# Performance work log

Hardware: AMD Instinct MI355X
Metric: run time of the kernel (lower is better)

Reference implementation:

```python
import jax, jax.numpy as jnp
import numpy as np

B, D_IN, D_H, W_RANK, U_RANK = 8192, 1024, 2048, 256, 256


def setup_inputs() -> dict:
    key = jax.random.key(0)
    ks = jax.random.split(key, 6)
    return {
        "input": jax.random.normal(ks[0], (B, D_IN), dtype=jnp.float32),
        "state": jax.random.normal(ks[1], (B, D_H), dtype=jnp.float32),
        "W1": 0.1 * jax.random.normal(ks[2], (W_RANK, D_IN), dtype=jnp.float32),
        "W2": 0.1 * jax.random.normal(ks[3], (D_H, W_RANK), dtype=jnp.float32),
        "U1": 0.1 * jax.random.normal(ks[4], (U_RANK, D_H), dtype=jnp.float32),
        "U2": 0.1 * jax.random.normal(ks[5], (D_H, U_RANK), dtype=jnp.float32),
        "bias_gate": jnp.ones((1, D_H), dtype=jnp.float32),
        "bias_update": jnp.ones((1, D_H), dtype=jnp.float32),
        "zeta": 1.0 * jnp.ones((1, 1), dtype=jnp.float32),
        "nu": -4.0 * jnp.ones((1, 1), dtype=jnp.float32),
    }


def reference(input, state, W1, W2, U1, U2, bias_gate, bias_update, zeta, nu):
    # Low-rank projections: Wx = x @ W1^T @ W2^T ; Uh = h @ U1^T @ U2^T
    wx = jnp.einsum("bi,ri->br", input, W1)          # [B, wRank]
    wx = jnp.einsum("br,hr->bh", wx, W2)             # [B, H]
    uh = jnp.einsum("bh,rh->br", state, U1)          # [B, uRank]
    uh = jnp.einsum("br,hr->bh", uh, U2)             # [B, H]
    pre = wx + uh                                     # shared pre-activation
    z = jax.nn.sigmoid(pre + bias_gate)               # gate (sigmoid)
    h_cand = jnp.tanh(pre + bias_update)              # update (tanh)
    # h_t = z*h_{t-1} + (sigmoid(zeta)*(1-z) + sigmoid(nu)) * h_cand
    new_h = z * state + (jax.nn.sigmoid(zeta) * (1.0 - z) + jax.nn.sigmoid(nu)) * h_cand
    return new_h
```

## Files before the change

### kernel.cpp

```cpp
#include <hip/hip_runtime.h>
#include <hip/hip_fp16.h>
#include <cstdint>
#include <cstddef>


typedef _Float16 half8 __attribute__((ext_vector_type(8)));
typedef float f32x4 __attribute__((ext_vector_type(4)));

#define DIN 1024
#define DH 2048
#define RK 256
#define RBLD 768
#define OFF_W1H 0
#define OFF_U1H 262144
#define OFF_W2H 786432
#define OFF_U2H 1310720
#define WB_HALVES 1835008

__device__ __forceinline__ half8 cvt8(const float4 a, const float4 b) {
  half8 h;
  h[0] = (_Float16)a.x; h[1] = (_Float16)a.y; h[2] = (_Float16)a.z; h[3] = (_Float16)a.w;
  h[4] = (_Float16)b.x; h[5] = (_Float16)b.y; h[6] = (_Float16)b.z; h[7] = (_Float16)b.w;
  return h;
}

__global__ __launch_bounds__(256)
void fgrnn_prep(const float* __restrict__ W1, const float* __restrict__ U1,
                const float* __restrict__ W2, const float* __restrict__ U2,
                _Float16* __restrict__ wb) {
  const int q = blockIdx.x * 256 + threadIdx.x;
  const float* src;
  int rel;
  if (q < 65536) { src = W1; rel = q; }
  else if (q < 196608) { src = U1; rel = q - 65536; }
  else if (q < 327680) { src = W2; rel = q - 196608; }
  else { src = U2; rel = q - 327680; }
  const float4 v = reinterpret_cast<const float4*>(src)[rel];
  union { _Float16 h[4]; uint2 u; } cv;
  cv.h[0] = (_Float16)v.x; cv.h[1] = (_Float16)v.y;
  cv.h[2] = (_Float16)v.z; cv.h[3] = (_Float16)v.w;
  reinterpret_cast<uint2*>(wb)[q] = cv.u;
}

template <int MI>
__device__ __forceinline__ void s1_body(
    const float* __restrict__ A, const int KA, const int kbase,
    const _Float16* __restrict__ Bw, _Float16* __restrict__ rbuf,
    const int row0, const int colbase,
    _Float16* __restrict__ AsBase, _Float16* __restrict__ BsBase) {
  constexpr int APASS = MI / 2;
  constexpr int ASTRIDE = MI * 32 * 64;
  constexpr int BSTRIDE = 256 * 64;

  const int tid = threadIdx.x;
  const int lane = tid & 63;
  const int w = tid >> 6;
  const int wr = w >> 2, wc = w & 3;
  const int sr = tid >> 3;
  const int sc = (tid & 7) * 8;

  f32x4 acc[MI][4];
#pragma unroll
  for (int i = 0; i < MI; ++i)
#pragma unroll
    for (int j = 0; j < 4; ++j) acc[i][j] = (f32x4){0.f, 0.f, 0.f, 0.f};

  float4 raE[APASS][2], raO[APASS][2];
  half8 rbE[4], rbO[4];

  auto LOADG = [&](float4 (&ra)[APASS][2], half8 (&rb)[4], int it) {
    const int k0 = kbase + it * 64;
#pragma unroll
    for (int j = 0; j < APASS; ++j) {
      const float* s = A + (size_t)(row0 + j * 64 + sr) * KA + k0 + sc;
      ra[j][0] = *reinterpret_cast<const float4*>(s);
      ra[j][1] = *reinterpret_cast<const float4*>(s + 4);
    }
#pragma unroll
    for (int j = 0; j < 4; ++j)
      rb[j] = *reinterpret_cast<const half8*>(Bw + (size_t)(j * 64 + sr) * KA + k0 + sc);
  };
  auto STORE = [&](const float4 (&ra)[APASS][2], const half8 (&rb)[4],
                   _Float16* as, _Float16* bs) {
#pragma unroll
    for (int j = 0; j < APASS; ++j) {
      const int r = j * 64 + sr;
      *reinterpret_cast<half8*>(&as[r * 64 + (sc ^ ((r & 7) << 3))]) =
          cvt8(ra[j][0], ra[j][1]);
    }
#pragma unroll
    for (int j = 0; j < 4; ++j) {
      const int r = j * 64 + sr;
      *reinterpret_cast<half8*>(&bs[r * 64 + (sc ^ ((r & 7) << 3))]) = rb[j];
    }
  };
  auto COMPUTE = [&](const _Float16* as, const _Float16* bs) {
#pragma unroll
    for (int kk = 0; kk < 64; kk += 32) {
      half8 af[MI], bf[4];
#pragma unroll
      for (int mi = 0; mi < MI; ++mi) {
        const int r = wr * (MI * 16) + mi * 16 + (lane & 15);
        af[mi] = *reinterpret_cast<const half8*>(
            &as[r * 64 + ((kk + 8 * (lane >> 4)) ^ ((r & 7) << 3))]);
      }
#pragma unroll
      for (int ni = 0; ni < 4; ++ni) {
        const int r = wc * 64 + ni * 16 + (lane & 15);
        bf[ni] = *reinterpret_cast<const half8*>(
            &bs[r * 64 + ((kk + 8 * (lane >> 4)) ^ ((r & 7) << 3))]);
      }
#pragma unroll
      for (int mi = 0; mi < MI; ++mi)
#pragma unroll
        for (int ni = 0; ni < 4; ++ni)
          acc[mi][ni] =
              __builtin_amdgcn_mfma_f32_16x16x32_f16(af[mi], bf[ni], acc[mi][ni], 0, 0, 0);
    }
  };
  auto BAR = [&]() {
    asm volatile("s_waitcnt lgkmcnt(0)" ::: "memory");
    __builtin_amdgcn_s_barrier();
    asm volatile("" ::: "memory");
  };

  _Float16* as0 = AsBase;
  _Float16* as1 = AsBase + ASTRIDE;
  _Float16* bs0 = BsBase;
  _Float16* bs1 = BsBase + BSTRIDE;

  LOADG(raE, rbE, 0);
  LOADG(raO, rbO, 1);
  STORE(raE, rbE, as0, bs0);
  BAR();

#pragma unroll 1
  for (int it2 = 0; it2 < 16; it2 += 2) {
    if (it2 + 2 < 16) LOADG(raE, rbE, it2 + 2);
    COMPUTE(as0, bs0);
    STORE(raO, rbO, as1, bs1);
    BAR();
    if (it2 + 3 < 16) LOADG(raO, rbO, it2 + 3);
    COMPUTE(as1, bs1);
    if (it2 + 2 < 16) STORE(raE, rbE, as0, bs0);
    BAR();
  }

#pragma unroll
  for (int mi = 0; mi < MI; ++mi)
#pragma unroll
    for (int ni = 0; ni < 4; ++ni)
#pragma unroll
      for (int e = 0; e < 4; ++e) {
        const int row = row0 + wr * (MI * 16) + mi * 16 + 4 * (lane >> 4) + e;
        const int col = colbase + wc * 64 + ni * 16 + (lane & 15);
        rbuf[(size_t)row * RBLD + col] = (_Float16)acc[mi][ni][e];
      }
}

__global__ __launch_bounds__(512)
void fgrnn_stage1(const float* __restrict__ x, const float* __restrict__ h,
                  const _Float16* __restrict__ wb, _Float16* __restrict__ rbuf) {
  __shared__ _Float16 As[2 * 128 * 64];
  __shared__ _Float16 Bs[2 * 256 * 64];
  const int bid = blockIdx.x;
  if (bid < 128) {
    s1_body<2>(x, DIN, 0, wb + OFF_W1H, rbuf, bid * 64, 0, As, Bs);
  } else if (bid < 192) {
    s1_body<4>(h, DH, 0, wb + OFF_U1H, rbuf, (bid - 128) * 128, 256, As, Bs);
  } else {
    s1_body<4>(h, DH, 1024, wb + OFF_U1H, rbuf, (bid - 192) * 128, 512, As, Bs);
  }
}

__global__ __launch_bounds__(256)
void fgrnn_stage2(const _Float16* __restrict__ rbuf, const _Float16* __restrict__ wb,
                  const float* __restrict__ state,
                  const float* __restrict__ bg, const float* __restrict__ bu,
                  const float* __restrict__ zeta, const float* __restrict__ nu,
                  float* __restrict__ out) {
  const int bid = blockIdx.x;
  const int L = (bid & 7) * 256 + (bid >> 3);
  const int mtile = L >> 4;
  const int ntile = L & 15;
  const int row0 = mtile * 64;
  const int col0 = ntile * 128;
  const _Float16* W2h = wb + OFF_W2H;
  const _Float16* U2h = wb + OFF_U2H;

  __shared__ _Float16 As[64 * 64];
  __shared__ _Float16 Bs[128 * 64];

  const int tid = threadIdx.x;
  const int lane = tid & 63;
  const int w = tid >> 6;
  const int wr = w >> 1, wc = w & 1;

  f32x4 acc[2][4];
#pragma unroll
  for (int i = 0; i < 2; ++i)
#pragma unroll
    for (int j = 0; j < 4; ++j) acc[i][j] = (f32x4){0.f, 0.f, 0.f, 0.f};

  const int sr = tid >> 3;
  const int sc = (tid & 7) * 8;

  half8 pa[2], pa2[2], pb[4];

  auto LOADG = [&](int it) {
    const int k0 = it * 64;
    const bool iswx = (k0 < 256);
#pragma unroll
    for (int j = 0; j < 2; ++j) {
      const _Float16* p = rbuf + (size_t)(row0 + j * 32 + sr) * RBLD + k0 + sc;
      pa[j] = *reinterpret_cast<const half8*>(p);
      if (!iswx) pa2[j] = *reinterpret_cast<const half8*>(p + 256);
    }
    const _Float16* Bh = iswx ? W2h : U2h;
    const int kb = k0 & 255;
#pragma unroll
    for (int j = 0; j < 4; ++j)
      pb[j] = *reinterpret_cast<const half8*>(Bh + (size_t)(col0 + j * 32 + sr) * RK + kb + sc);
  };
  auto STORE = [&](int it) {
    const int k0 = it * 64;
#pragma unroll
    for (int j = 0; j < 2; ++j) {
      half8 v = pa[j];
      if (k0 >= 256) v = v + pa2[j];
      const int r = j * 32 + sr;
      *reinterpret_cast<half8*>(&As[r * 64 + (sc ^ ((r & 7) << 3))]) = v;
    }
#pragma unroll
    for (int j = 0; j < 4; ++j) {
      const int r = j * 32 + sr;
      *reinterpret_cast<half8*>(&Bs[r * 64 + (sc ^ ((r & 7) << 3))]) = pb[j];
    }
  };

  LOADG(0);
  STORE(0);
  __syncthreads();

  for (int it = 0; it < 8; ++it) {
    const bool more = (it + 1 < 8);
    if (more) LOADG(it + 1);
#pragma unroll
    for (int kk = 0; kk < 64; kk += 32) {
      half8 af[2], bf[4];
#pragma unroll
      for (int mi = 0; mi < 2; ++mi) {
        const int r = wr * 32 + mi * 16 + (lane & 15);
        af[mi] = *reinterpret_cast<const half8*>(
            &As[r * 64 + ((kk + 8 * (lane >> 4)) ^ ((r & 7) << 3))]);
      }
#pragma unroll
      for (int ni = 0; ni < 4; ++ni) {
        const int r = wc * 64 + ni * 16 + (lane & 15);
        bf[ni] = *reinterpret_cast<const half8*>(
            &Bs[r * 64 + ((kk + 8 * (lane >> 4)) ^ ((r & 7) << 3))]);
      }
#pragma unroll
      for (int mi = 0; mi < 2; ++mi)
#pragma unroll
        for (int ni = 0; ni < 4; ++ni)
          acc[mi][ni] =
              __builtin_amdgcn_mfma_f32_16x16x32_f16(af[mi], bf[ni], acc[mi][ni], 0, 0, 0);
    }
    if (more) {
      __syncthreads();
      STORE(it + 1);
    }
    __syncthreads();
  }

  const float LOG2E = 1.44269504f;
  const float sz = __builtin_amdgcn_rcpf(1.f + __builtin_amdgcn_exp2f(-zeta[0] * LOG2E));
  const float sn = __builtin_amdgcn_rcpf(1.f + __builtin_amdgcn_exp2f(-nu[0] * LOG2E));
#pragma unroll
  for (int mi = 0; mi < 2; ++mi)
#pragma unroll
    for (int ni = 0; ni < 4; ++ni) {
      const int col = col0 + wc * 64 + ni * 16 + (lane & 15);
      const float bgc = bg[col];
      const float buc = bu[col];
#pragma unroll
      for (int e = 0; e < 4; ++e) {
        const int row = row0 + wr * 32 + mi * 16 + 4 * (lane >> 4) + e;
        const float pre = acc[mi][ni][e];
        const float zg =
            __builtin_amdgcn_rcpf(1.f + __builtin_amdgcn_exp2f(-(pre + bgc) * LOG2E));
        const float hc =
            1.f - 2.f * __builtin_amdgcn_rcpf(
                            1.f + __builtin_amdgcn_exp2f((pre + buc) * (2.f * LOG2E)));
        const float sv = state[(size_t)row * DH + col];
        out[(size_t)row * DH + col] = zg * sv + (sz * (1.f - zg) + sn) * hc;
      }
    }
}

extern "C" void kernel_launch(void* const* d_in, const int* in_sizes, int n_in,
                              void* d_out, int out_size, void* d_ws, size_t ws_size,
                              hipStream_t stream) {
  const float* input = (const float*)d_in[0];
  const float* state = (const float*)d_in[1];
  const float* W1 = (const float*)d_in[2];
  const float* W2 = (const float*)d_in[3];
  const float* U1 = (const float*)d_in[4];
  const float* U2 = (const float*)d_in[5];
  const float* bg = (const float*)d_in[6];
  const float* bu = (const float*)d_in[7];
  const float* zeta = (const float*)d_in[8];
  const float* nu = (const float*)d_in[9];
  float* out = (float*)d_out;

  _Float16* rbuf = (_Float16*)d_ws;
  _Float16* wb = rbuf + (size_t)8192 * RBLD;

  fgrnn_prep<<<1792, 256, 0, stream>>>(W1, U1, W2, U2, wb);
  fgrnn_stage1<<<256, 512, 0, stream>>>(input, state, wb, rbuf);
  fgrnn_stage2<<<2048, 256, 0, stream>>>(rbuf, wb, state, bg, bu, zeta, nu, out);
}
```

Before: 69.03 us.

## Retile stage-1 GEMM into uniform 64x128 tiles with more, smaller blocks

Stage 1 previously ran 256 blocks of 512 threads, and their tiles were unequal in size (64-row blocks for x, 128-row blocks for h). It now launches 768 uniform 256-thread blocks, each computing a 64x128 output tile. A swizzled block index groups blocks across XCDs. The aim is to fill all CUs evenly and allow several blocks per CU, at the cost of re-reading the A rows once per 128-column half.

```diff
diff --git a/kernel.cpp b/kernel.cpp
--- a/kernel.cpp
+++ b/kernel.cpp
@@ -15,7 +15,6 @@
 #define OFF_U1H 262144
 #define OFF_W2H 786432
 #define OFF_U2H 1310720
-#define WB_HALVES 1835008
 
 __device__ __forceinline__ half8 cvt8(const float4 a, const float4 b) {
   half8 h;
@@ -42,65 +41,75 @@
   reinterpret_cast<uint2*>(wb)[q] = cv.u;
 }
 
-template <int MI>
-__device__ __forceinline__ void s1_body(
-    const float* __restrict__ A, const int KA, const int kbase,
-    const _Float16* __restrict__ Bw, _Float16* __restrict__ rbuf,
-    const int row0, const int colbase,
-    _Float16* __restrict__ AsBase, _Float16* __restrict__ BsBase) {
-  constexpr int APASS = MI / 2;
-  constexpr int ASTRIDE = MI * 32 * 64;
-  constexpr int BSTRIDE = 256 * 64;
+__global__ __launch_bounds__(256, 3)
+void fgrnn_stage1(const float* __restrict__ x, const float* __restrict__ h,
+                  const _Float16* __restrict__ wb, _Float16* __restrict__ rbuf) {
+  __shared__ _Float16 As[2 * 64 * 64];
+  __shared__ _Float16 Bs[2 * 128 * 64];
+
+  const int bid = blockIdx.x;
+  const int L = (bid & 7) * 96 + (bid >> 3);
+  const int g = L >> 8;
+  const int rem = L & 255;
+  const int ncol = rem >> 7;
+  const int mtile = rem & 127;
+  const bool isx = (g == 0);
+  const float* A = isx ? x : h;
+  const int KA = isx ? DIN : DH;
+  const int kbase = (g == 2) ? 1024 : 0;
+  const _Float16* Bw = wb + (isx ? OFF_W1H : OFF_U1H) + (size_t)(ncol * 128) * KA;
+  const int row0 = mtile * 64;
+  const int colbase = g * 256 + ncol * 128;
 
   const int tid = threadIdx.x;
   const int lane = tid & 63;
   const int w = tid >> 6;
-  const int wr = w >> 2, wc = w & 3;
+  const int wr = w >> 1, wc = w & 1;
   const int sr = tid >> 3;
   const int sc = (tid & 7) * 8;
 
-  f32x4 acc[MI][4];
-#pragma unroll
-  for (int i = 0; i < MI; ++i)
+  f32x4 acc[2][4];
+#pragma unroll
+  for (int i = 0; i < 2; ++i)
 #pragma unroll
     for (int j = 0; j < 4; ++j) acc[i][j] = (f32x4){0.f, 0.f, 0.f, 0.f};
 
-  float4 raE[APASS][2], raO[APASS][2];
+  float4 raE[2][2], raO[2][2];
   half8 rbE[4], rbO[4];
 
-  auto LOADG = [&](float4 (&ra)[APASS][2], half8 (&rb)[4], int it) {
+  auto LOADG = [&](float4 (&ra)[2][2], half8 (&rb)[4], int it) {
     const int k0 = kbase + it * 64;
 #pragma unroll
-    for (int j = 0; j < APASS; ++j) {
-      const float* s = A + (size_t)(row0 + j * 64 + sr) * KA + k0 + sc;
+    for (int j = 0; j < 2; ++j) {
+      const float* s = A + (size_t)(row0 + j * 32 + sr) * KA + k0 + sc;
       ra[j][0] = *reinterpret_cast<const float4*>(s);
       ra[j][1] = *reinterpret_cast<const float4*>(s + 4);
     }
 #pragma unroll
     for (int j = 0; j < 4; ++j)
-      rb[j] = *reinterpret_cast<const half8*>(Bw + (size_t)(j * 64 + sr) * KA + k0 + sc);
-  };
-  auto STORE = [&](const float4 (&ra)[APASS][2], const half8 (&rb)[4],
+      rb[j] = *reinterpret_cast<const half8*>(Bw + (size_t)(j * 32 + sr) * KA + k0 + sc);
+  };
+  auto STORE = [&](const float4 (&ra)[2][2], const half8 (&rb)[4],
                    _Float16* as, _Float16* bs) {
 #pragma unroll
-    for (int j = 0; j < APASS; ++j) {
-      const int r = j * 64 + sr;
+    for (int j = 0; j < 2; ++j) {
+      const int r = j * 32 + sr;
       *reinterpret_cast<half8*>(&as[r * 64 + (sc ^ ((r & 7) << 3))]) =
           cvt8(ra[j][0], ra[j][1]);
     }
 #pragma unroll
     for (int j = 0; j < 4; ++j) {
-      const int r = j * 64 + sr;
+      const int r = j * 32 + sr;
       *reinterpret_cast<half8*>(&bs[r * 64 + (sc ^ ((r & 7) << 3))]) = rb[j];
     }
   };
   auto COMPUTE = [&](const _Float16* as, const _Float16* bs) {
 #pragma unroll
     for (int kk = 0; kk < 64; kk += 32) {
-      half8 af[MI], bf[4];
-#pragma unroll
-      for (int mi = 0; mi < MI; ++mi) {
-        const int r = wr * (MI * 16) + mi * 16 + (lane & 15);
+      half8 af[2], bf[4];
+#pragma unroll
+      for (int mi = 0; mi < 2; ++mi) {
+        const int r = wr * 32 + mi * 16 + (lane & 15);
         af[mi] = *reinterpret_cast<const half8*>(
             &as[r * 64 + ((kk + 8 * (lane >> 4)) ^ ((r & 7) << 3))]);
       }
@@ -111,7 +120,7 @@
             &bs[r * 64 + ((kk + 8 * (lane >> 4)) ^ ((r & 7) << 3))]);
       }
 #pragma unroll
-      for (int mi = 0; mi < MI; ++mi)
+      for (int mi = 0; mi < 2; ++mi)
 #pragma unroll
         for (int ni = 0; ni < 4; ++ni)
           acc[mi][ni] =
@@ -124,10 +133,10 @@
     asm volatile("" ::: "memory");
   };
 
-  _Float16* as0 = AsBase;
-  _Float16* as1 = AsBase + ASTRIDE;
-  _Float16* bs0 = BsBase;
-  _Float16* bs1 = BsBase + BSTRIDE;
+  _Float16* as0 = As;
+  _Float16* as1 = As + 64 * 64;
+  _Float16* bs0 = Bs;
+  _Float16* bs1 = Bs + 128 * 64;
 
   LOADG(raE, rbE, 0);
   LOADG(raO, rbO, 1);
@@ -147,30 +156,15 @@
   }
 
 #pragma unroll
-  for (int mi = 0; mi < MI; ++mi)
+  for (int mi = 0; mi < 2; ++mi)
 #pragma unroll
     for (int ni = 0; ni < 4; ++ni)
 #pragma unroll
       for (int e = 0; e < 4; ++e) {
-        const int row = row0 + wr * (MI * 16) + mi * 16 + 4 * (lane >> 4) + e;
+        const int row = row0 + wr * 32 + mi * 16 + 4 * (lane >> 4) + e;
         const int col = colbase + wc * 64 + ni * 16 + (lane & 15);
         rbuf[(size_t)row * RBLD + col] = (_Float16)acc[mi][ni][e];
       }
-}
-
-__global__ __launch_bounds__(512)
-void fgrnn_stage1(const float* __restrict__ x, const float* __restrict__ h,
-                  const _Float16* __restrict__ wb, _Float16* __restrict__ rbuf) {
-  __shared__ _Float16 As[2 * 128 * 64];
-  __shared__ _Float16 Bs[2 * 256 * 64];
-  const int bid = blockIdx.x;
-  if (bid < 128) {
-    s1_body<2>(x, DIN, 0, wb + OFF_W1H, rbuf, bid * 64, 0, As, Bs);
-  } else if (bid < 192) {
-    s1_body<4>(h, DH, 0, wb + OFF_U1H, rbuf, (bid - 128) * 128, 256, As, Bs);
-  } else {
-    s1_body<4>(h, DH, 1024, wb + OFF_U1H, rbuf, (bid - 192) * 128, 512, As, Bs);
-  }
 }
 
 __global__ __launch_bounds__(256)
@@ -318,6 +312,6 @@
   _Float16* wb = rbuf + (size_t)8192 * RBLD;
 
   fgrnn_prep<<<1792, 256, 0, stream>>>(W1, U1, W2, U2, wb);
-  fgrnn_stage1<<<256, 512, 0, stream>>>(input, state, wb, rbuf);
+  fgrnn_stage1<<<768, 256, 0, stream>>>(input, state, wb, rbuf);
   fgrnn_stage2<<<2048, 256, 0, stream>>>(rbuf, wb, state, bg, bu, zeta, nu, out);
 }
```

Measured after the change: 78.64 us. 1.14x slower.

## Use direct global-to-LDS loads for weights and double-buffer both GEMM stages

Applied to the files above, without the earlier changes.

Weight tiles in both stages now go straight from global memory into LDS through global_load_lds, so they no longer pass through registers. Stage 2 gains double-buffered LDS with one barrier per iteration in place of two syncthreads. Stage 1 is retiled so each block covers 128 output columns over more rows (8 waves laid out 4x2), and the register pipeline is simplified to a single buffer. Wave priority is raised around the MFMA compute. The aim is less register pressure and fewer stalls on loads and barriers, but each iteration now waits on vmcnt(0), which may expose global load latency.

```diff
diff --git a/kernel.cpp b/kernel.cpp
--- a/kernel.cpp
+++ b/kernel.cpp
@@ -15,13 +15,18 @@
 #define OFF_U1H 262144
 #define OFF_W2H 786432
 #define OFF_U2H 1310720
-#define WB_HALVES 1835008
 
 __device__ __forceinline__ half8 cvt8(const float4 a, const float4 b) {
   half8 h;
   h[0] = (_Float16)a.x; h[1] = (_Float16)a.y; h[2] = (_Float16)a.z; h[3] = (_Float16)a.w;
   h[4] = (_Float16)b.x; h[5] = (_Float16)b.y; h[6] = (_Float16)b.z; h[7] = (_Float16)b.w;
   return h;
+}
+
+__device__ __forceinline__ void gload16(const _Float16* g, _Float16* lds) {
+  __builtin_amdgcn_global_load_lds(
+      (const __attribute__((address_space(1))) unsigned*)g,
+      (__attribute__((address_space(3))) unsigned*)lds, 16, 0, 0);
 }
 
 __global__ __launch_bounds__(256)
@@ -47,15 +52,13 @@
     const float* __restrict__ A, const int KA, const int kbase,
     const _Float16* __restrict__ Bw, _Float16* __restrict__ rbuf,
     const int row0, const int colbase,
-    _Float16* __restrict__ AsBase, _Float16* __restrict__ BsBase) {
-  constexpr int APASS = MI / 2;
-  constexpr int ASTRIDE = MI * 32 * 64;
-  constexpr int BSTRIDE = 256 * 64;
+    _Float16* __restrict__ AsB, _Float16* __restrict__ BsB) {
+  constexpr int ASTR = MI * 64 * 64;
 
   const int tid = threadIdx.x;
   const int lane = tid & 63;
-  const int w = tid >> 6;
-  const int wr = w >> 2, wc = w & 3;
+  const int wv = tid >> 6;
+  const int wr = wv >> 1, wc = wv & 1;
   const int sr = tid >> 3;
   const int sc = (tid & 7) * 8;
 
@@ -65,33 +68,33 @@
 #pragma unroll
     for (int j = 0; j < 4; ++j) acc[i][j] = (f32x4){0.f, 0.f, 0.f, 0.f};
 
-  float4 raE[APASS][2], raO[APASS][2];
-  half8 rbE[4], rbO[4];
-
-  auto LOADG = [&](float4 (&ra)[APASS][2], half8 (&rb)[4], int it) {
+  float4 ra[MI][2];
+
+  auto LOADA = [&](int it) {
     const int k0 = kbase + it * 64;
 #pragma unroll
-    for (int j = 0; j < APASS; ++j) {
+    for (int j = 0; j < MI; ++j) {
       const float* s = A + (size_t)(row0 + j * 64 + sr) * KA + k0 + sc;
       ra[j][0] = *reinterpret_cast<const float4*>(s);
       ra[j][1] = *reinterpret_cast<const float4*>(s + 4);
     }
-#pragma unroll
-    for (int j = 0; j < 4; ++j)
-      rb[j] = *reinterpret_cast<const half8*>(Bw + (size_t)(j * 64 + sr) * KA + k0 + sc);
-  };
-  auto STORE = [&](const float4 (&ra)[APASS][2], const half8 (&rb)[4],
-                   _Float16* as, _Float16* bs) {
-#pragma unroll
-    for (int j = 0; j < APASS; ++j) {
+  };
+  auto GLOADB = [&](_Float16* bs, int it) {
+    const int k0 = kbase + it * 64;
+#pragma unroll
+    for (int g = 0; g < 2; ++g) {
+      const int rb = wv * 16 + g * 8;
+      const int row = rb + (lane >> 3);
+      const int ch = ((lane & 7) * 8) ^ ((row & 7) << 3);
+      gload16(Bw + (size_t)row * KA + k0 + ch, bs + rb * 64);
+    }
+  };
+  auto STOREA = [&](_Float16* as) {
+#pragma unroll
+    for (int j = 0; j < MI; ++j) {
       const int r = j * 64 + sr;
       *reinterpret_cast<half8*>(&as[r * 64 + (sc ^ ((r & 7) << 3))]) =
           cvt8(ra[j][0], ra[j][1]);
-    }
-#pragma unroll
-    for (int j = 0; j < 4; ++j) {
-      const int r = j * 64 + sr;
-      *reinterpret_cast<half8*>(&bs[r * 64 + (sc ^ ((r & 7) << 3))]) = rb[j];
     }
   };
   auto COMPUTE = [&](const _Float16* as, const _Float16* bs) {
@@ -118,32 +121,37 @@
               __builtin_amdgcn_mfma_f32_16x16x32_f16(af[mi], bf[ni], acc[mi][ni], 0, 0, 0);
     }
   };
-  auto BAR = [&]() {
+
+  _Float16* as0 = AsB;
+  _Float16* as1 = AsB + ASTR;
+  _Float16* bs0 = BsB;
+  _Float16* bs1 = BsB + 128 * 64;
+
+  LOADA(0);
+  GLOADB(bs0, 0);
+  STOREA(as0);
+  asm volatile("s_waitcnt vmcnt(0)" ::: "memory");
+  asm volatile("s_waitcnt lgkmcnt(0)" ::: "memory");
+  __builtin_amdgcn_s_barrier();
+  __builtin_amdgcn_sched_barrier(0);
+
+  int p = 0;
+#pragma unroll 1
+  for (int it = 0; it < 16; ++it) {
+    const bool more = (it + 1 < 16);
+    if (more) {
+      LOADA(it + 1);
+      GLOADB(p ? bs0 : bs1, it + 1);
+    }
+    __builtin_amdgcn_s_setprio(1);
+    COMPUTE(p ? as1 : as0, p ? bs1 : bs0);
+    __builtin_amdgcn_s_setprio(0);
+    if (more) STOREA(p ? as0 : as1);
+    asm volatile("s_waitcnt vmcnt(0)" ::: "memory");
     asm volatile("s_waitcnt lgkmcnt(0)" ::: "memory");
     __builtin_amdgcn_s_barrier();
-    asm volatile("" ::: "memory");
-  };
-
-  _Float16* as0 = AsBase;
-  _Float16* as1 = AsBase + ASTRIDE;
-  _Float16* bs0 = BsBase;
-  _Float16* bs1 = BsBase + BSTRIDE;
-
-  LOADG(raE, rbE, 0);
-  LOADG(raO, rbO, 1);
-  STORE(raE, rbE, as0, bs0);
-  BAR();
-
-#pragma unroll 1
-  for (int it2 = 0; it2 < 16; it2 += 2) {
-    if (it2 + 2 < 16) LOADG(raE, rbE, it2 + 2);
-    COMPUTE(as0, bs0);
-    STORE(raO, rbO, as1, bs1);
-    BAR();
-    if (it2 + 3 < 16) LOADG(raO, rbO, it2 + 3);
-    COMPUTE(as1, bs1);
-    if (it2 + 2 < 16) STORE(raE, rbE, as0, bs0);
-    BAR();
+    __builtin_amdgcn_sched_barrier(0);
+    p ^= 1;
   }
 
 #pragma unroll
@@ -161,15 +169,21 @@
 __global__ __launch_bounds__(512)
 void fgrnn_stage1(const float* __restrict__ x, const float* __restrict__ h,
                   const _Float16* __restrict__ wb, _Float16* __restrict__ rbuf) {
-  __shared__ _Float16 As[2 * 128 * 64];
-  __shared__ _Float16 Bs[2 * 256 * 64];
+  __shared__ _Float16 As[2 * 256 * 64];
+  __shared__ _Float16 Bs[2 * 128 * 64];
   const int bid = blockIdx.x;
   if (bid < 128) {
-    s1_body<2>(x, DIN, 0, wb + OFF_W1H, rbuf, bid * 64, 0, As, Bs);
-  } else if (bid < 192) {
-    s1_body<4>(h, DH, 0, wb + OFF_U1H, rbuf, (bid - 128) * 128, 256, As, Bs);
+    const int mtile = bid >> 1;
+    const int ncol = bid & 1;
+    s1_body<2>(x, DIN, 0, wb + OFF_W1H + (size_t)(ncol * 128) * DIN, rbuf,
+               mtile * 128, ncol * 128, As, Bs);
   } else {
-    s1_body<4>(h, DH, 1024, wb + OFF_U1H, rbuf, (bid - 192) * 128, 512, As, Bs);
+    const int t = bid - 128;
+    const int mtile = t >> 2;
+    const int kp = (t >> 1) & 1;
+    const int ncol = t & 1;
+    s1_body<4>(h, DH, kp * 1024, wb + OFF_U1H + (size_t)(ncol * 128) * DH, rbuf,
+               mtile * 256, 256 + kp * 256 + ncol * 128, As, Bs);
   }
 }
 
@@ -188,26 +202,25 @@
   const _Float16* W2h = wb + OFF_W2H;
   const _Float16* U2h = wb + OFF_U2H;
 
-  __shared__ _Float16 As[64 * 64];
-  __shared__ _Float16 Bs[128 * 64];
+  __shared__ _Float16 As[2 * 64 * 64];
+  __shared__ _Float16 Bs[2 * 128 * 64];
 
   const int tid = threadIdx.x;
   const int lane = tid & 63;
-  const int w = tid >> 6;
-  const int wr = w >> 1, wc = w & 1;
-
-  f32x4 acc[2][4];
-#pragma unroll
-  for (int i = 0; i < 2; ++i)
-#pragma unroll
-    for (int j = 0; j < 4; ++j) acc[i][j] = (f32x4){0.f, 0.f, 0.f, 0.f};
-
+  const int wv = tid >> 6;
+  const int wr = wv >> 1, wc = wv & 1;
   const int sr = tid >> 3;
   const int sc = (tid & 7) * 8;
 
-  half8 pa[2], pa2[2], pb[4];
-
-  auto LOADG = [&](int it) {
+  f32x4 acc[2][4];
+#pragma unroll
+  for (int i = 0; i < 2; ++i)
+#pragma unroll
+    for (int j = 0; j < 4; ++j) acc[i][j] = (f32x4){0.f, 0.f, 0.f, 0.f};
+
+  half8 pa[2], pa2[2];
+
+  auto LOADA = [&](int it) {
     const int k0 = it * 64;
     const bool iswx = (k0 < 256);
 #pragma unroll
@@ -216,35 +229,30 @@
       pa[j] = *reinterpret_cast<const half8*>(p);
       if (!iswx) pa2[j] = *reinterpret_cast<const half8*>(p + 256);
     }
-    const _Float16* Bh = iswx ? W2h : U2h;
+  };
+  auto GLOADB = [&](_Float16* bs, int it) {
+    const int k0 = it * 64;
+    const _Float16* Bh = (k0 < 256) ? W2h : U2h;
     const int kb = k0 & 255;
 #pragma unroll
-    for (int j = 0; j < 4; ++j)
-      pb[j] = *reinterpret_cast<const half8*>(Bh + (size_t)(col0 + j * 32 + sr) * RK + kb + sc);
-  };
-  auto STORE = [&](int it) {
+    for (int g = 0; g < 4; ++g) {
+      const int rb = wv * 32 + g * 8;
+      const int row = rb + (lane >> 3);
+      const int ch = ((lane & 7) * 8) ^ ((row & 7) << 3);
+      gload16(Bh + (size_t)(col0 + row) * RK + kb + ch, bs + rb * 64);
+    }
+  };
+  auto STOREA = [&](_Float16* as, int it) {
     const int k0 = it * 64;
 #pragma unroll
     for (int j = 0; j < 2; ++j) {
       half8 v = pa[j];
       if (k0 >= 256) v = v + pa2[j];
       const int r = j * 32 + sr;
-      *reinterpret_cast<half8*>(&As[r * 64 + (sc ^ ((r & 7) << 3))]) = v;
-    }
-#pragma unroll
-    for (int j = 0; j < 4; ++j) {
-      const int r = j * 32 + sr;
-      *reinterpret_cast<half8*>(&Bs[r * 64 + (sc ^ ((r & 7) << 3))]) = pb[j];
-    }
-  };
-
-  LOADG(0);
-  STORE(0);
-  __syncthreads();
-
-  for (int it = 0; it < 8; ++it) {
-    const bool more = (it + 1 < 8);
-    if (more) LOADG(it + 1);
+      *reinterpret_cast<half8*>(&as[r * 64 + (sc ^ ((r & 7) << 3))]) = v;
+    }
+  };
+  auto COMPUTE = [&](const _Float16* as, const _Float16* bs) {
 #pragma unroll
     for (int kk = 0; kk < 64; kk += 32) {
       half8 af[2], bf[4];
@@ -252,13 +260,13 @@
       for (int mi = 0; mi < 2; ++mi) {
         const int r = wr * 32 + mi * 16 + (lane & 15);
         af[mi] = *reinterpret_cast<const half8*>(
-            &As[r * 64 + ((kk + 8 * (lane >> 4)) ^ ((r & 7) << 3))]);
+            &as[r * 64 + ((kk + 8 * (lane >> 4)) ^ ((r & 7) << 3))]);
       }
 #pragma unroll
       for (int ni = 0; ni < 4; ++ni) {
         const int r = wc * 64 + ni * 16 + (lane & 15);
         bf[ni] = *reinterpret_cast<const half8*>(
-            &Bs[r * 64 + ((kk + 8 * (lane >> 4)) ^ ((r & 7) << 3))]);
+            &bs[r * 64 + ((kk + 8 * (lane >> 4)) ^ ((r & 7) << 3))]);
       }
 #pragma unroll
       for (int mi = 0; mi < 2; ++mi)
@@ -267,11 +275,38 @@
           acc[mi][ni] =
               __builtin_amdgcn_mfma_f32_16x16x32_f16(af[mi], bf[ni], acc[mi][ni], 0, 0, 0);
     }
+  };
+
+  _Float16* as0 = As;
+  _Float16* as1 = As + 64 * 64;
+  _Float16* bs0 = Bs;
+  _Float16* bs1 = Bs + 128 * 64;
+
+  LOADA(0);
+  GLOADB(bs0, 0);
+  STOREA(as0, 0);
+  asm volatile("s_waitcnt vmcnt(0)" ::: "memory");
+  asm volatile("s_waitcnt lgkmcnt(0)" ::: "memory");
+  __builtin_amdgcn_s_barrier();
+  __builtin_amdgcn_sched_barrier(0);
+
+  int p = 0;
+#pragma unroll 1
+  for (int it = 0; it < 8; ++it) {
+    const bool more = (it + 1 < 8);
     if (more) {
-      __syncthreads();
-      STORE(it + 1);
-    }
-    __syncthreads();
+      LOADA(it + 1);
+      GLOADB(p ? bs0 : bs1, it + 1);
+    }
+    __builtin_amdgcn_s_setprio(1);
+    COMPUTE(p ? as1 : as0, p ? bs1 : bs0);
+    __builtin_amdgcn_s_setprio(0);
+    if (more) STOREA(p ? as0 : as1, it + 1);
+    asm volatile("s_waitcnt vmcnt(0)" ::: "memory");
+    asm volatile("s_waitcnt lgkmcnt(0)" ::: "memory");
+    __builtin_amdgcn_s_barrier();
+    __builtin_amdgcn_sched_barrier(0);
+    p ^= 1;
   }
 
   const float LOG2E = 1.44269504f;
```

After: 84.74 us. 1.23x slower.
